# Kernel optimization log

Hardware: AMD Instinct MI355X
Metric: run time of the kernel (lower is better)

## Reference

```python
import jax, jax.numpy as jnp
import numpy as np

SKIP = 2 ** -0.5
EPS = 1e-6
DIM = 1024
N_LAYERS = 8
N_HEADS = 16
MAX_SEQ = 1024
B = 4
L = 1024


def get_rot_emb(dim, max_seq_len):
    pos = jnp.arange(max_seq_len, dtype=jnp.float32)
    omega = 1.0 / 10000.0 ** (jnp.arange(0, dim, 2, dtype=jnp.float32) / dim)
    angles = pos[:, None] * omega[None, :]  # [S, dim/2]
    cos = jnp.repeat(jnp.cos(angles), 2, axis=-1)  # [S, dim]
    sin = jnp.repeat(jnp.sin(angles), 2, axis=-1)
    return cos, sin


def setup_inputs() -> dict:
    key = jax.random.key(0)
    ks = jax.random.split(key, 16)
    s = 0.02
    d = DIM
    nl = N_LAYERS
    cos, sin = get_rot_emb(d // N_HEADS, MAX_SEQ)
    inp = {
        'x': jax.random.normal(ks[0], (B, L, d), jnp.float32),
        'c': jax.random.normal(ks[1], (B, 1, d), jnp.float32),
        't': jax.random.normal(ks[2], (B, d), jnp.float32),
        'num_heads': N_HEADS,
        'cos': cos,
        'sin': sin,
        'qkv_w': jax.random.normal(ks[3], (nl, d, 3 * d), jnp.float32) * s,
        'qkv_b': jnp.zeros((nl, 3 * d), jnp.float32),
        'proj_w': jax.random.normal(ks[4], (nl, d, d), jnp.float32) * s,
        'proj_b': jnp.zeros((nl, d), jnp.float32),
        'mlp_w1': jax.random.normal(ks[5], (nl, d, 4 * d), jnp.float32) * s,
        'mlp_b1': jnp.zeros((nl, 4 * d), jnp.float32),
        'mlp_w2': jax.random.normal(ks[6], (nl, 4 * d, d), jnp.float32) * s,
        'mlp_b2': jnp.zeros((nl, d), jnp.float32),
        'adaln_w': jax.random.normal(ks[7], (nl, d, 6 * d), jnp.float32) * s,
        'adaln_b': jnp.zeros((nl, 6 * d), jnp.float32),
    }
    return inp


def layer_norm(x):
    mu = jnp.mean(x, axis=-1, keepdims=True)
    var = jnp.var(x, axis=-1, keepdims=True)
    return (x - mu) * jax.lax.rsqrt(var + EPS)


def rotate_half(q):
    # torch: stack([-q[..., 1::2], q[..., ::2]], -1).reshape(q.shape)
    q2 = q.reshape(q.shape[:-1] + (-1, 2))
    return jnp.stack([-q2[..., 1], q2[..., 0]], axis=-1).reshape(q.shape)


def reference(x, c, t, num_heads, cos, sin, qkv_w, qkv_b, proj_w, proj_b, mlp_w1, mlp_b1, mlp_w2, mlp_b2, adaln_w, adaln_b):
    Bx, Lx, C = x.shape
    H = int(num_heads)
    D = C // H
    scale = D ** -0.5
    cmod = (c + t[:, None]) * SKIP  # [B,1,C]
    cos_l = cos[:Lx]  # [L,D]
    sin_l = sin[:Lx]

    def block(xcur, p):
        qw, qb, pw, pb, w1, b1, w2, b2, aw, ab = p
        mod = jax.nn.silu(cmod) @ aw + ab  # [B,1,6C]
        sh1, sc1, g1, sh2, sc2, g2 = jnp.split(mod, 6, axis=-1)
        h = (layer_norm(xcur) * (1 + sc1) + sh1) * SKIP
        qkv = (h @ qw + qb).reshape(Bx, Lx, 3, H, D).transpose(2, 0, 3, 1, 4)
        q, k, v = qkv[0], qkv[1], qkv[2]  # [B,H,L,D]
        q = q * cos_l + rotate_half(q) * sin_l
        k = k * cos_l + rotate_half(k) * sin_l
        attn = jax.nn.softmax(scale * jnp.einsum('bhid,bhjd->bhij', q, k), axis=-1)
        o = jnp.einsum('bhij,bhjd->bhid', attn, v).transpose(0, 2, 1, 3).reshape(Bx, Lx, C)
        o = o @ pw + pb
        xcur = (xcur + g1 * o) * SKIP
        h2 = (layer_norm(xcur) * (1 + sc2) + sh2) * SKIP
        m = jax.nn.gelu(h2 @ w1 + b1, approximate=True) @ w2 + b2
        return (xcur + g2 * m) * SKIP, None

    params = (qkv_w, qkv_b, proj_w, proj_b, mlp_w1, mlp_b1, mlp_w2, mlp_b2, adaln_w, adaln_b)
    out, _ = jax.lax.scan(block, x, params)
    return out
```

## Files before the change

### kernel.cpp

```cpp
#include <hip/hip_runtime.h>

#define SKIPF 0.70710678118654752440f

typedef unsigned short u16;
typedef unsigned int u32;
typedef __attribute__((ext_vector_type(4))) short bf16x4;
typedef __attribute__((ext_vector_type(8))) short bf16x8;
typedef __attribute__((ext_vector_type(4))) float f32x4;

#define MFMA32(A, B, C) __builtin_amdgcn_mfma_f32_16x16x32_bf16(A, B, C, 0, 0, 0)
#define MFMA16(A, B, C) __builtin_amdgcn_mfma_f32_16x16x16bf16_1k(A, B, C, 0, 0, 0)

__device__ __forceinline__ float bf2f(u16 v) {
  u32 u = ((u32)v) << 16; float f; __builtin_memcpy(&f, &u, 4); return f;
}
__device__ __forceinline__ u16 f2bf(float f) {
  u32 u; __builtin_memcpy(&u, &f, 4);
  u = (u + 0x7fffu + ((u >> 16) & 1u)) >> 16;
  return (u16)u;
}
__device__ __forceinline__ void gload16(const void* g, void* s) {
  __builtin_amdgcn_global_load_lds((const __attribute__((address_space(1))) void*)g,
                                   (__attribute__((address_space(3))) void*)s, 16, 0, 0);
}


__global__ void silu_prep_kernel(const float* __restrict__ c, const float* __restrict__ t,
                                 float* __restrict__ silu_c) {
  int i = blockIdx.x * 256 + threadIdx.x;
  float x = (c[i] + t[i]) * SKIPF;
  silu_c[i] = x / (1.f + __expf(-x));
}

__global__ void adaln_part_kernel(const float* __restrict__ silu_c, const float* __restrict__ aw,
                                  float* __restrict__ part) {
  __shared__ float sc[4][64];
  int n = blockIdx.x * 256 + threadIdx.x;
  int ks = blockIdx.y;
  int k0 = ks * 64;
  int b = threadIdx.x >> 6, kk = threadIdx.x & 63;
  sc[b][kk] = silu_c[b * 1024 + k0 + kk];
  __syncthreads();
  float a0 = 0.f, a1 = 0.f, a2 = 0.f, a3 = 0.f;
  for (int k = 0; k < 64; ++k) {
    float w = aw[(size_t)(k0 + k) * 6144 + n];
    a0 += sc[0][k] * w; a1 += sc[1][k] * w; a2 += sc[2][k] * w; a3 += sc[3][k] * w;
  }
  part[(size_t)(ks * 4 + 0) * 6144 + n] = a0;
  part[(size_t)(ks * 4 + 1) * 6144 + n] = a1;
  part[(size_t)(ks * 4 + 2) * 6144 + n] = a2;
  part[(size_t)(ks * 4 + 3) * 6144 + n] = a3;
}

__global__ void adaln_reduce_kernel(const float* __restrict__ part, const float* __restrict__ ab,
                                    float* __restrict__ mod) {
  int i = blockIdx.x * 256 + threadIdx.x;
  int b = i / 6144, n = i - b * 6144;
  float a = ab[n];
  for (int ks = 0; ks < 16; ++ks) a += part[(size_t)(ks * 4 + b) * 6144 + n];
  mod[(size_t)b * 6144 + n] = a;
}

__global__ void wtrans4_kernel(const float* __restrict__ wq, u16* __restrict__ oq,
                               const float* __restrict__ wp, u16* __restrict__ op,
                               const float* __restrict__ w1p, u16* __restrict__ o1,
                               const float* __restrict__ w2p, u16* __restrict__ o2) {
  __shared__ float tile[32][33];
  int bid = blockIdx.x;
  const float* W; u16* WT; int nx, K, N, base;
  if (bid < 3072)      { W = wq;  WT = oq; nx = 96;  K = 1024; N = 3072; base = 0; }
  else if (bid < 4096) { W = wp;  WT = op; nx = 32;  K = 1024; N = 1024; base = 3072; }
  else if (bid < 8192) { W = w1p; WT = o1; nx = 128; K = 1024; N = 4096; base = 4096; }
  else                 { W = w2p; WT = o2; nx = 32;  K = 4096; N = 1024; base = 8192; }
  int t = bid - base;
  int n0 = (t % nx) * 32, k0 = (t / nx) * 32;
  int tx = threadIdx.x, ty = threadIdx.y;
#pragma unroll
  for (int i = 0; i < 4; ++i)
    tile[ty * 4 + i][tx] = W[(size_t)(k0 + ty * 4 + i) * N + n0 + tx];
  __syncthreads();
#pragma unroll
  for (int i = 0; i < 4; ++i)
    WT[(size_t)(n0 + ty * 4 + i) * K + k0 + tx] = f2bf(tile[tx][ty * 4 + i]);
}

__global__ __launch_bounds__(256) void ln_mod_kernel(const float* __restrict__ xin,
                                                     const float* __restrict__ mod,
                                                     u16* __restrict__ h, int sh_off, int sc_off) {
  int row = blockIdx.x;
  int b = row >> 10;
  const float4* xr = (const float4*)(xin + (size_t)row * 1024);
  float4 v = xr[threadIdx.x];
  float s = v.x + v.y + v.z + v.w;
  float ss = v.x * v.x + v.y * v.y + v.z * v.z + v.w * v.w;
#pragma unroll
  for (int o = 32; o; o >>= 1) { s += __shfl_xor(s, o); ss += __shfl_xor(ss, o); }
  __shared__ float red[8];
  int wave = threadIdx.x >> 6;
  if ((threadIdx.x & 63) == 0) { red[wave * 2] = s; red[wave * 2 + 1] = ss; }
  __syncthreads();
  s = red[0] + red[2] + red[4] + red[6];
  ss = red[1] + red[3] + red[5] + red[7];
  float mu = s * (1.f / 1024.f);
  float var = ss * (1.f / 1024.f) - mu * mu;
  float rs = rsqrtf(var + 1e-6f);
  int n = threadIdx.x * 4;
  const float* mb = mod + (size_t)b * 6144;
  float4 sc = *(const float4*)(mb + sc_off + n);
  float4 sh = *(const float4*)(mb + sh_off + n);
  ushort4 o4;
  o4.x = f2bf(((v.x - mu) * rs * (1.f + sc.x) + sh.x) * SKIPF);
  o4.y = f2bf(((v.y - mu) * rs * (1.f + sc.y) + sh.y) * SKIPF);
  o4.z = f2bf(((v.z - mu) * rs * (1.f + sc.z) + sh.z) * SKIPF);
  o4.w = f2bf(((v.w - mu) * rs * (1.f + sc.w) + sh.w) * SKIPF);
  *(ushort4*)(h + (size_t)row * 1024 + n) = o4;
}

template <int EPI>
__global__ __launch_bounds__(512, 1) void gemm256r_kernel(
    const u16* __restrict__ A, const u16* __restrict__ BT, const float* __restrict__ bias,
    u16* __restrict__ Cb, int NBX, int N, int K) {
  __shared__ u16 lds[4][16384];
  const int tid = threadIdx.x;
  const int lane = tid & 63, wave = tid >> 6;
  const int lq = lane & 15, lk = lane >> 4;
  const int wr = wave >> 2, wc = wave & 3;

  int per = gridDim.x >> 3;
  int swz = (blockIdx.x & 7) * per + (blockIdx.x >> 3);
  int bx = swz % NBX, by = swz / NBX;
  const int m0 = by * 256, n0 = bx * 256;

  f32x4 acc[8][4];
#pragma unroll
  for (int i = 0; i < 8; ++i)
#pragma unroll
    for (int j = 0; j < 4; ++j) acc[i][j] = (f32x4){0.f, 0.f, 0.f, 0.f};

  auto STAGE = [&](int slot, int t) {
    int kt = t * 32;
    char* Ab = (char*)lds[slot];
    char* Bb = (char*)(lds[slot] + 8192);
#pragma unroll
    for (int q = 0; q < 2; ++q) {
      int u = tid + q * 512;
      int r = u >> 3, cpos = u & 7;
      int g = cpos ^ (r & 7);
      gload16(A + (size_t)(m0 + 2 * r + (g >> 2)) * K + kt + (g & 3) * 8, Ab + u * 16);
    }
#pragma unroll
    for (int q = 0; q < 2; ++q) {
      int u = tid + q * 512;
      int r = u >> 3, cpos = u & 7;
      int g = cpos ^ (r & 7);
      gload16(BT + (size_t)(n0 + 2 * r + (g >> 2)) * K + kt + (g & 3) * 8, Bb + u * 16);
    }
  };

  const int NT = K >> 5;
  STAGE(0, 0); STAGE(1, 1); STAGE(2, 2);
  int slot = 0;
  for (int t = 0; t < NT; ++t) {
    int rem = NT - 1 - t;
    if (rem >= 2) asm volatile("s_waitcnt vmcnt(8)" ::: "memory");
    else if (rem == 1) asm volatile("s_waitcnt vmcnt(4)" ::: "memory");
    else asm volatile("s_waitcnt vmcnt(0)" ::: "memory");
    __builtin_amdgcn_s_barrier();
    __builtin_amdgcn_sched_barrier(0);
    if (t + 3 < NT) { int ns = slot + 3; if (ns >= 4) ns -= 4; STAGE(ns, t + 3); }
    const char* Ab = (const char*)lds[slot];
    const char* Bb = (const char*)(lds[slot] + 8192);
    bf16x8 bfr[4];
#pragma unroll
    for (int ni = 0; ni < 4; ++ni) {
      int nrow = wc * 64 + ni * 16 + lq;
      int r = nrow >> 1, g = (nrow & 1) * 4 + lk;
      bfr[ni] = *(const bf16x8*)(Bb + r * 128 + ((g ^ (r & 7)) << 4));
    }
#pragma unroll
    for (int ph = 0; ph < 4; ++ph) {
      bf16x8 af0, af1;
      {
        int mrow = wr * 128 + (ph * 2) * 16 + lq;
        int r = mrow >> 1, g = (mrow & 1) * 4 + lk;
        af0 = *(const bf16x8*)(Ab + r * 128 + ((g ^ (r & 7)) << 4));
        mrow += 16;
        r = mrow >> 1; g = (mrow & 1) * 4 + lk;
        af1 = *(const bf16x8*)(Ab + r * 128 + ((g ^ (r & 7)) << 4));
      }
      __builtin_amdgcn_s_setprio(1);
#pragma unroll
      for (int j = 0; j < 4; ++j) acc[ph * 2][j] = MFMA32(af0, bfr[j], acc[ph * 2][j]);
#pragma unroll
      for (int j = 0; j < 4; ++j) acc[ph * 2 + 1][j] = MFMA32(af1, bfr[j], acc[ph * 2 + 1][j]);
      __builtin_amdgcn_s_setprio(0);
    }
    ++slot; if (slot >= 4) slot = 0;
  }

#pragma unroll
  for (int i = 0; i < 8; ++i) {
    int rbase = m0 + wr * 128 + i * 16 + lk * 4;
#pragma unroll
    for (int j = 0; j < 4; ++j) {
      int cg = n0 + wc * 64 + j * 16 + lq;
      float bv = bias[cg];
#pragma unroll
      for (int r = 0; r < 4; ++r) {
        int row = rbase + r;
        float val = acc[i][j][r] + bv;
        if (EPI == 0) {
          Cb[(size_t)row * N + cg] = f2bf(val);
        } else {
          float tt = 0.7978845608028654f * (val + 0.044715f * val * val * val);
          float e = __expf(2.f * tt);
          float th = 1.f - 2.f / (e + 1.f);
          Cb[(size_t)row * N + cg] = f2bf(0.5f * val * (1.f + th));
        }
      }
    }
  }
}

__global__ __launch_bounds__(256) void gemm_res_kernel(
    const u16* __restrict__ A, const u16* __restrict__ BT, const float* __restrict__ bias,
    const float* __restrict__ xin, float* __restrict__ xout, const float* __restrict__ mod,
    int g_off, int K) {
  __shared__ u16 As[3][64 * 32];
  __shared__ u16 Bs[3][128 * 32];
  const int tid = threadIdx.x;
  const int lane = tid & 63, wave = tid >> 6;
  const int lq = lane & 15, lk = lane >> 4;
  const int wr = wave >> 1, wc = wave & 1;
  const int m0 = blockIdx.x * 64, n0 = blockIdx.y * 128;

  const int srow = tid >> 2;
  const int skc = (tid & 3) * 8;
  const u16* Ag = A + (size_t)(m0 + srow) * K + skc;
  const u16* Bg = BT + (size_t)(n0 + srow) * K + skc;

  f32x4 acc[2][4];
#pragma unroll
  for (int i = 0; i < 2; ++i)
#pragma unroll
    for (int j = 0; j < 4; ++j) acc[i][j] = (f32x4){0.f, 0.f, 0.f, 0.f};

  auto STAGE = [&](int slot, int t) {
    int kt = t * 32;
    gload16(Ag + kt, (char*)As[slot] + tid * 16);
    gload16(Bg + kt, (char*)Bs[slot] + tid * 16);
    gload16(Bg + (size_t)64 * K + kt, (char*)Bs[slot] + 4096 + tid * 16);
  };

  const int NT = K >> 5;
  STAGE(0, 0); STAGE(1, 1);
  int slot = 0;
  for (int t = 0; t < NT; ++t) {
    if (t + 1 < NT) asm volatile("s_waitcnt vmcnt(3)" ::: "memory");
    else asm volatile("s_waitcnt vmcnt(0)" ::: "memory");
    __builtin_amdgcn_s_barrier();
    __builtin_amdgcn_sched_barrier(0);
    if (t + 2 < NT) { int ns = slot + 2; if (ns >= 3) ns -= 3; STAGE(ns, t + 2); }
    const bf16x8* Av = (const bf16x8*)As[slot];
    const bf16x8* Bv = (const bf16x8*)Bs[slot];
    bf16x8 af[2], bfr[4];
#pragma unroll
    for (int i = 0; i < 2; ++i) af[i] = Av[(wr * 32 + i * 16 + lq) * 4 + lk];
#pragma unroll
    for (int j = 0; j < 4; ++j) bfr[j] = Bv[(wc * 64 + j * 16 + lq) * 4 + lk];
    __builtin_amdgcn_s_setprio(1);
#pragma unroll
    for (int i = 0; i < 2; ++i)
#pragma unroll
      for (int j = 0; j < 4; ++j) acc[i][j] = MFMA32(af[i], bfr[j], acc[i][j]);
    __builtin_amdgcn_s_setprio(0);
    ++slot; if (slot >= 3) slot = 0;
  }

#pragma unroll
  for (int i = 0; i < 2; ++i) {
    int rbase = m0 + wr * 32 + i * 16 + lk * 4;
#pragma unroll
    for (int j = 0; j < 4; ++j) {
      int cg = n0 + wc * 64 + j * 16 + lq;
      float bv = bias[cg];
#pragma unroll
      for (int r = 0; r < 4; ++r) {
        int row = rbase + r;
        float val = acc[i][j][r] + bv;
        int b = row >> 10;
        float g = mod[(size_t)b * 6144 + g_off + cg];
        float xv = xin[(size_t)row * 1024 + cg];
        xout[(size_t)row * 1024 + cg] = (xv + g * val) * SKIPF;
      }
    }
  }
}

__global__ __launch_bounds__(256) void ropev_kernel(
    const u16* __restrict__ qkv, const float* __restrict__ cosb, const float* __restrict__ sinb,
    u16* __restrict__ qo, u16* __restrict__ ko, u16* __restrict__ vt) {
  __shared__ u16 tile[64][72];
  int bh = blockIdx.y, l0 = blockIdx.x * 64;
  int b = bh >> 4, h = bh & 15;
  int r = threadIdx.x >> 2, c = (threadIdx.x & 3) * 16;
  int l = l0 + r;
  const u16* src = qkv + (size_t)(b * 1024 + l) * 3072 + h * 64 + c;
  *(uint4*)&tile[r][c] = *(const uint4*)(src + 2048);
  *(uint4*)&tile[r][c + 8] = *(const uint4*)(src + 2048 + 8);
  size_t dst_off = ((size_t)bh * 1024 + l) * 64 + c;
#pragma unroll
  for (int qk = 0; qk < 2; ++qk) {
    const u16* s2 = src + qk * 1024;
    u32 w0[4], w1[4];
#pragma unroll
    for (int p = 0; p < 8; ++p) {
      u32 pr = *(const u32*)(s2 + p * 2);
      int d0 = c + p * 2;
      float cc = cosb[l * 64 + d0], sn = sinb[l * 64 + d0];
      float e0 = bf2f((u16)(pr & 0xffff)), e1 = bf2f((u16)(pr >> 16));
      u32 ow = (u32)f2bf(e0 * cc - e1 * sn) | ((u32)f2bf(e1 * cc + e0 * sn) << 16);
      if (p < 4) w0[p] = ow; else w1[p - 4] = ow;
    }
    u16* dst = (qk ? ko : qo) + dst_off;
    uint4 v0; v0.x = w0[0]; v0.y = w0[1]; v0.z = w0[2]; v0.w = w0[3];
    uint4 v1; v1.x = w1[0]; v1.y = w1[1]; v1.z = w1[2]; v1.w = w1[3];
    *(uint4*)dst = v0;
    *(uint4*)(dst + 8) = v1;
  }
  __syncthreads();
  int d = threadIdx.x >> 2, lc = threadIdx.x & 3;
  u16 tmp[16];
#pragma unroll
  for (int j = 0; j < 16; ++j) tmp[j] = tile[lc * 16 + j][d];
  u16* dstv = vt + ((size_t)bh * 64 + d) * 1024 + l0 + lc * 16;
  *(uint4*)dstv = *(uint4*)tmp;
  *(uint4*)(dstv + 8) = *(uint4*)(tmp + 8);
}

__global__ __launch_bounds__(256) void attn_kernel(const u16* __restrict__ qb,
                                                   const u16* __restrict__ kb,
                                                   const u16* __restrict__ vt,
                                                   u16* __restrict__ ob) {
  __shared__ u16 ktile[3][4096];
  __shared__ u16 vtile[3][4096];
  int nid = (blockIdx.x & 7) * 64 + (blockIdx.x >> 3);
  int qt = nid & 7, bh = nid >> 3;
  int tid = threadIdx.x;
  int lane = tid & 63, wave = tid >> 6;
  int lq = lane & 15, lk = lane >> 4;
  const u16* Q = qb + (size_t)bh * 65536;
  const u16* Kp = kb + (size_t)bh * 65536;
  const u16* VT = vt + (size_t)bh * 65536;
  int qbase = qt * 128 + wave * 32;

  bf16x8 qf[2][2];
#pragma unroll
  for (int g = 0; g < 2; ++g) {
    qf[g][0] = *(const bf16x8*)(Q + (size_t)(qbase + g * 16 + lq) * 64 + lk * 8);
    qf[g][1] = *(const bf16x8*)(Q + (size_t)(qbase + g * 16 + lq) * 64 + 32 + lk * 8);
  }

  auto stage_one = [&](int buf, int kvb, int u) {
    int r = u >> 3;
    int cc = ((u & 7) ^ (r & 7)) * 8;
    gload16(Kp + (size_t)(kvb + r) * 64 + cc, (char*)ktile[buf] + u * 16);
    gload16(VT + (size_t)r * 1024 + kvb + cc, (char*)vtile[buf] + u * 16);
  };

  float mrun[2] = {-1e30f, -1e30f}, lsum[2] = {0.f, 0.f};
  f32x4 oacc[2][4];
#pragma unroll
  for (int g = 0; g < 2; ++g)
#pragma unroll
    for (int f = 0; f < 4; ++f) oacc[g][f] = (f32x4){0.f, 0.f, 0.f, 0.f};
  const f32x4 z4 = (f32x4){0.f, 0.f, 0.f, 0.f};

  stage_one(0, 0, tid); stage_one(0, 0, tid + 256);
  stage_one(1, 64, tid); stage_one(1, 64, tid + 256);
  int slot = 0;
  for (int t = 0; t < 16; ++t) {
    if (t < 15) asm volatile("s_waitcnt vmcnt(4)" ::: "memory");
    else asm volatile("s_waitcnt vmcnt(0)" ::: "memory");
    __builtin_amdgcn_s_barrier();
    __builtin_amdgcn_sched_barrier(0);
    if (t + 2 < 16) {
      int ns = slot + 2; if (ns >= 3) ns -= 3;
      stage_one(ns, (t + 2) * 64, tid);
      stage_one(ns, (t + 2) * 64, tid + 256);
    }
    const char* kb_ = (const char*)ktile[slot];
    const char* vb_ = (const char*)vtile[slot];
    f32x4 st[2][4];
    __builtin_amdgcn_s_setprio(1);
#pragma unroll
    for (int s = 0; s < 4; ++s) {
      int r = s * 16 + lq;
      int sw = (r & 7) << 4;
      bf16x8 kf0 = *(const bf16x8*)(kb_ + r * 128 + ((lk * 16) ^ sw));
      bf16x8 kf1 = *(const bf16x8*)(kb_ + r * 128 + ((64 + lk * 16) ^ sw));
      st[0][s] = MFMA32(kf0, qf[0][0], z4);
      st[0][s] = MFMA32(kf1, qf[0][1], st[0][s]);
      st[1][s] = MFMA32(kf0, qf[1][0], z4);
      st[1][s] = MFMA32(kf1, qf[1][1], st[1][s]);
    }
    __builtin_amdgcn_s_setprio(0);
    bf16x4 pf[2][4];
#pragma unroll
    for (int g = 0; g < 2; ++g) {
      float pm = -1e30f;
#pragma unroll
      for (int s = 0; s < 4; ++s)
#pragma unroll
        for (int r = 0; r < 4; ++r) {
          st[g][s][r] *= 0.125f;
          pm = fmaxf(pm, st[g][s][r]);
        }
      pm = fmaxf(pm, __shfl_xor(pm, 16));
      pm = fmaxf(pm, __shfl_xor(pm, 32));
      if (!__all(pm - mrun[g] <= 8.f)) {
        float mnew = fmaxf(mrun[g], pm);
        float corr = __expf(mrun[g] - mnew);
        float c0 = __shfl(corr, lk * 4 + 0), c1 = __shfl(corr, lk * 4 + 1);
        float c2 = __shfl(corr, lk * 4 + 2), c3 = __shfl(corr, lk * 4 + 3);
#pragma unroll
        for (int f = 0; f < 4; ++f) {
          oacc[g][f][0] *= c0; oacc[g][f][1] *= c1;
          oacc[g][f][2] *= c2; oacc[g][f][3] *= c3;
        }
        lsum[g] *= corr;
        mrun[g] = mnew;
      }
      float ps = 0.f;
#pragma unroll
      for (int s = 0; s < 4; ++s) {
        float p0 = __expf(st[g][s][0] - mrun[g]);
        float p1 = __expf(st[g][s][1] - mrun[g]);
        float p2 = __expf(st[g][s][2] - mrun[g]);
        float p3 = __expf(st[g][s][3] - mrun[g]);
        ps += p0 + p1 + p2 + p3;
        pf[g][s][0] = (short)f2bf(p0); pf[g][s][1] = (short)f2bf(p1);
        pf[g][s][2] = (short)f2bf(p2); pf[g][s][3] = (short)f2bf(p3);
      }
      ps += __shfl_xor(ps, 16);
      ps += __shfl_xor(ps, 32);
      lsum[g] += ps;
    }
    __builtin_amdgcn_s_setprio(1);
#pragma unroll
    for (int f = 0; f < 4; ++f) {
      int r = lq + f * 16;
      int sw = (r & 7) << 4;
#pragma unroll
      for (int s = 0; s < 4; ++s) {
        bf16x4 vf = *(const bf16x4*)(vb_ + r * 128 + ((s * 32 + lk * 8) ^ sw));
        oacc[0][f] = MFMA16(pf[0][s], vf, oacc[0][f]);
        oacc[1][f] = MFMA16(pf[1][s], vf, oacc[1][f]);
      }
    }
    __builtin_amdgcn_s_setprio(0);
    ++slot; if (slot >= 3) slot = 0;
  }

  int b = bh >> 4, hh = bh & 15;
#pragma unroll
  for (int g = 0; g < 2; ++g) {
    float inv = 1.f / lsum[g];
    float i0 = __shfl(inv, lk * 4 + 0), i1 = __shfl(inv, lk * 4 + 1);
    float i2 = __shfl(inv, lk * 4 + 2), i3 = __shfl(inv, lk * 4 + 3);
#pragma unroll
    for (int f = 0; f < 4; ++f) {
#pragma unroll
      for (int j = 0; j < 4; ++j) {
        int qrow = qbase + g * 16 + lk * 4 + j;
        float sc = (j == 0) ? i0 : (j == 1) ? i1 : (j == 2) ? i2 : i3;
        ob[((size_t)(b * 1024 + qrow)) * 1024 + hh * 64 + lq + f * 16] = f2bf(oacc[g][f][j] * sc);
      }
    }
  }
}


extern "C" void kernel_launch(void* const* d_in, const int* in_sizes, int n_in,
                              void* d_out, int out_size, void* d_ws, size_t ws_size,
                              hipStream_t stream) {
  const float* x = (const float*)d_in[0];
  const float* c = (const float*)d_in[1];
  const float* t = (const float*)d_in[2];
  const float* cosb = (const float*)d_in[4];
  const float* sinb = (const float*)d_in[5];
  const float* qkv_w = (const float*)d_in[6];
  const float* qkv_b = (const float*)d_in[7];
  const float* proj_w = (const float*)d_in[8];
  const float* proj_b = (const float*)d_in[9];
  const float* w1 = (const float*)d_in[10];
  const float* b1 = (const float*)d_in[11];
  const float* w2 = (const float*)d_in[12];
  const float* b2 = (const float*)d_in[13];
  const float* aw = (const float*)d_in[14];
  const float* ab = (const float*)d_in[15];

  constexpr size_t OFF_X = 0;
  constexpr size_t OFF_H = OFF_X + 16777216;
  constexpr size_t OFF_BIG = OFF_H + 8388608;
  constexpr size_t OFF_Q = OFF_BIG + 33554432;
  constexpr size_t OFF_K = OFF_Q + 8388608;
  constexpr size_t OFF_V = OFF_K + 8388608;
  constexpr size_t OFF_AO = OFF_V + 8388608;
  constexpr size_t OFF_WQ = OFF_AO + 8388608;
  constexpr size_t OFF_WP = OFF_WQ + 6291456;
  constexpr size_t OFF_W1 = OFF_WP + 2097152;
  constexpr size_t OFF_W2 = OFF_W1 + 8388608;
  constexpr size_t OFF_SC = OFF_W2 + 8388608;
  constexpr size_t OFF_MOD = OFF_SC + 16384;
  constexpr size_t OFF_PART = OFF_MOD + 98304;

  char* ws = (char*)d_ws;
  float* x_cur = (float*)(ws + OFF_X);
  u16* h = (u16*)(ws + OFF_H);
  u16* big = (u16*)(ws + OFF_BIG);
  u16* qv = (u16*)(ws + OFF_Q);
  u16* kv = (u16*)(ws + OFF_K);
  u16* vt = (u16*)(ws + OFF_V);
  u16* ao = (u16*)(ws + OFF_AO);
  u16* wTq = (u16*)(ws + OFF_WQ);
  u16* wTp = (u16*)(ws + OFF_WP);
  u16* wT1 = (u16*)(ws + OFF_W1);
  u16* wT2 = (u16*)(ws + OFF_W2);
  float* silu_c = (float*)(ws + OFF_SC);
  float* mod = (float*)(ws + OFF_MOD);
  float* part = (float*)(ws + OFF_PART);

  silu_prep_kernel<<<16, 256, 0, stream>>>(c, t, silu_c);

  for (int L = 0; L < 8; ++L) {
    const float* awL = aw + (size_t)L * 1024 * 6144;
    const float* abL = ab + (size_t)L * 6144;
    const float* qwL = qkv_w + (size_t)L * 1024 * 3072;
    const float* qbL = qkv_b + (size_t)L * 3072;
    const float* pwL = proj_w + (size_t)L * 1024 * 1024;
    const float* pbL = proj_b + (size_t)L * 1024;
    const float* w1L = w1 + (size_t)L * 1024 * 4096;
    const float* b1L = b1 + (size_t)L * 4096;
    const float* w2L = w2 + (size_t)L * 4096 * 1024;
    const float* b2L = b2 + (size_t)L * 1024;

    const float* xin = (L == 0) ? x : x_cur;
    float* xout2 = (L == 7) ? (float*)d_out : x_cur;

    adaln_part_kernel<<<dim3(24, 16), 256, 0, stream>>>(silu_c, awL, part);
    adaln_reduce_kernel<<<96, 256, 0, stream>>>(part, abL, mod);
    wtrans4_kernel<<<12288, dim3(32, 8), 0, stream>>>(qwL, wTq, pwL, wTp, w1L, wT1, w2L, wT2);

    ln_mod_kernel<<<4096, 256, 0, stream>>>(xin, mod, h, 0, 1024);
    gemm256r_kernel<0><<<192, 512, 0, stream>>>(h, wTq, qbL, big, 12, 3072, 1024);
    ropev_kernel<<<dim3(16, 64), 256, 0, stream>>>(big, cosb, sinb, qv, kv, vt);
    attn_kernel<<<512, 256, 0, stream>>>(qv, kv, vt, ao);
    gemm_res_kernel<<<dim3(64, 8), 256, 0, stream>>>(ao, wTp, pbL, xin, x_cur, mod, 2048, 1024);
    ln_mod_kernel<<<4096, 256, 0, stream>>>(x_cur, mod, h, 3072, 4096);
    gemm256r_kernel<1><<<256, 512, 0, stream>>>(h, wT1, b1L, big, 16, 4096, 1024);
    gemm_res_kernel<<<dim3(64, 8), 256, 0, stream>>>(big, wT2, b2L, x_cur, xout2, mod, 5120, 4096);
  }
}
```

Measured before the change: 2.142 ms.

## Enlarge residual GEMM tile to 128x128 with XOR-swizzled LDS layout

The residual-epilogue GEMM used for the attention projection and MLP down-projection now computes 128x128 output tiles per block instead of 64x128. Each wave accumulates a 64x64 region. The LDS staging uses an XOR swizzle over packed row pairs to avoid bank conflicts on fragment reads. This doubles operand reuse per block and halves the grid to 256 blocks, which may underfill the 256 CUs and increases register pressure.

Result: faster. 1.918 ms (-10.5%).

```diff
diff --git a/kernel.cpp b/kernel.cpp
--- a/kernel.cpp
+++ b/kernel.cpp
@@ -222,55 +222,64 @@
   }
 }
 
-__global__ __launch_bounds__(256) void gemm_res_kernel(
+__global__ __launch_bounds__(256) void gemm_res128_kernel(
     const u16* __restrict__ A, const u16* __restrict__ BT, const float* __restrict__ bias,
     const float* __restrict__ xin, float* __restrict__ xout, const float* __restrict__ mod,
     int g_off, int K) {
-  __shared__ u16 As[3][64 * 32];
-  __shared__ u16 Bs[3][128 * 32];
+  __shared__ u16 lds[3][8192];
   const int tid = threadIdx.x;
   const int lane = tid & 63, wave = tid >> 6;
   const int lq = lane & 15, lk = lane >> 4;
   const int wr = wave >> 1, wc = wave & 1;
-  const int m0 = blockIdx.x * 64, n0 = blockIdx.y * 128;
-
-  const int srow = tid >> 2;
-  const int skc = (tid & 3) * 8;
-  const u16* Ag = A + (size_t)(m0 + srow) * K + skc;
-  const u16* Bg = BT + (size_t)(n0 + srow) * K + skc;
-
-  f32x4 acc[2][4];
-#pragma unroll
-  for (int i = 0; i < 2; ++i)
+  const int m0 = blockIdx.x * 128, n0 = blockIdx.y * 128;
+
+  f32x4 acc[4][4];
+#pragma unroll
+  for (int i = 0; i < 4; ++i)
 #pragma unroll
     for (int j = 0; j < 4; ++j) acc[i][j] = (f32x4){0.f, 0.f, 0.f, 0.f};
 
   auto STAGE = [&](int slot, int t) {
     int kt = t * 32;
-    gload16(Ag + kt, (char*)As[slot] + tid * 16);
-    gload16(Bg + kt, (char*)Bs[slot] + tid * 16);
-    gload16(Bg + (size_t)64 * K + kt, (char*)Bs[slot] + 4096 + tid * 16);
+    char* Ab = (char*)lds[slot];
+    char* Bb = (char*)(lds[slot] + 4096);
+#pragma unroll
+    for (int q = 0; q < 2; ++q) {
+      int u = tid + q * 256;
+      int r = u >> 3, cpos = u & 7;
+      int g = cpos ^ (r & 7);
+      gload16(A + (size_t)(m0 + 2 * r + (g >> 2)) * K + kt + (g & 3) * 8, Ab + u * 16);
+      gload16(BT + (size_t)(n0 + 2 * r + (g >> 2)) * K + kt + (g & 3) * 8, Bb + u * 16);
+    }
   };
 
   const int NT = K >> 5;
   STAGE(0, 0); STAGE(1, 1);
   int slot = 0;
   for (int t = 0; t < NT; ++t) {
-    if (t + 1 < NT) asm volatile("s_waitcnt vmcnt(3)" ::: "memory");
+    if (t + 1 < NT) asm volatile("s_waitcnt vmcnt(4)" ::: "memory");
     else asm volatile("s_waitcnt vmcnt(0)" ::: "memory");
     __builtin_amdgcn_s_barrier();
     __builtin_amdgcn_sched_barrier(0);
     if (t + 2 < NT) { int ns = slot + 2; if (ns >= 3) ns -= 3; STAGE(ns, t + 2); }
-    const bf16x8* Av = (const bf16x8*)As[slot];
-    const bf16x8* Bv = (const bf16x8*)Bs[slot];
-    bf16x8 af[2], bfr[4];
-#pragma unroll
-    for (int i = 0; i < 2; ++i) af[i] = Av[(wr * 32 + i * 16 + lq) * 4 + lk];
-#pragma unroll
-    for (int j = 0; j < 4; ++j) bfr[j] = Bv[(wc * 64 + j * 16 + lq) * 4 + lk];
+    const char* Ab = (const char*)lds[slot];
+    const char* Bb = (const char*)(lds[slot] + 4096);
+    bf16x8 af[4], bfr[4];
+#pragma unroll
+    for (int i = 0; i < 4; ++i) {
+      int mrow = wr * 64 + i * 16 + lq;
+      int r = mrow >> 1, g = (mrow & 1) * 4 + lk;
+      af[i] = *(const bf16x8*)(Ab + r * 128 + ((g ^ (r & 7)) << 4));
+    }
+#pragma unroll
+    for (int j = 0; j < 4; ++j) {
+      int nrow = wc * 64 + j * 16 + lq;
+      int r = nrow >> 1, g = (nrow & 1) * 4 + lk;
+      bfr[j] = *(const bf16x8*)(Bb + r * 128 + ((g ^ (r & 7)) << 4));
+    }
     __builtin_amdgcn_s_setprio(1);
 #pragma unroll
-    for (int i = 0; i < 2; ++i)
+    for (int i = 0; i < 4; ++i)
 #pragma unroll
       for (int j = 0; j < 4; ++j) acc[i][j] = MFMA32(af[i], bfr[j], acc[i][j]);
     __builtin_amdgcn_s_setprio(0);
@@ -278,8 +287,8 @@
   }
 
 #pragma unroll
-  for (int i = 0; i < 2; ++i) {
-    int rbase = m0 + wr * 32 + i * 16 + lk * 4;
+  for (int i = 0; i < 4; ++i) {
+    int rbase = m0 + wr * 64 + i * 16 + lk * 4;
 #pragma unroll
     for (int j = 0; j < 4; ++j) {
       int cg = n0 + wc * 64 + j * 16 + lq;
@@ -556,9 +565,9 @@
     gemm256r_kernel<0><<<192, 512, 0, stream>>>(h, wTq, qbL, big, 12, 3072, 1024);
     ropev_kernel<<<dim3(16, 64), 256, 0, stream>>>(big, cosb, sinb, qv, kv, vt);
     attn_kernel<<<512, 256, 0, stream>>>(qv, kv, vt, ao);
-    gemm_res_kernel<<<dim3(64, 8), 256, 0, stream>>>(ao, wTp, pbL, xin, x_cur, mod, 2048, 1024);
+    gemm_res128_kernel<<<dim3(32, 8), 256, 0, stream>>>(ao, wTp, pbL, xin, x_cur, mod, 2048, 1024);
     ln_mod_kernel<<<4096, 256, 0, stream>>>(x_cur, mod, h, 3072, 4096);
     gemm256r_kernel<1><<<256, 512, 0, stream>>>(h, wT1, b1L, big, 16, 4096, 1024);
-    gemm_res_kernel<<<dim3(64, 8), 256, 0, stream>>>(big, wT2, b2L, x_cur, xout2, mod, 5120, 4096);
-  }
-}
+    gemm_res128_kernel<<<dim3(32, 8), 256, 0, stream>>>(big, wT2, b2L, x_cur, xout2, mod, 5120, 4096);
+  }
+}
```
